# Kernel tuning notes

Hardware: AMD Instinct MI355X
Metric: run time of the kernel (lower is better)

The kernel has to match this reference:

```python
import jax, jax.numpy as jnp
import numpy as np

C_FEAT = 512
HID = 256
OUT = 3
IN_DIM = C_FEAT + 2 + 2  # feat + rel_coord + rel_cell = 516


def _nearest_idx(g, size):
    # grid_sample nearest, align_corners=False: unnormalize then round (half-to-even)
    x = ((g + 1.0) * size - 1.0) / 2.0
    return jnp.clip(jnp.round(x).astype(jnp.int32), 0, size - 1)


def setup_inputs() -> dict:
    key = jax.random.key(0)
    ks = jax.random.split(key, 12)
    B, Q, H, W = 2, 65536, 48, 48
    feat = jax.random.normal(ks[0], (B, C_FEAT, H, W), dtype=jnp.float32)
    coord = jax.random.uniform(ks[1], (B, Q, 2), dtype=jnp.float32, minval=-1.0, maxval=1.0)
    cell = jnp.full((B, Q, 2), 2.0 / 256.0, dtype=jnp.float32)  # query at 256x256 output res
    def lin_init(k, fan_in, fan_out):
        s = 1.0 / np.sqrt(fan_in)
        return jax.random.uniform(k, (fan_in, fan_out), jnp.float32, -s, s)
    W0 = lin_init(ks[2], IN_DIM, HID); b0 = jnp.zeros((HID,), jnp.float32)
    W1 = lin_init(ks[3], HID, HID);    b1 = jnp.zeros((HID,), jnp.float32)
    W2 = lin_init(ks[4], HID, HID);    b2 = jnp.zeros((HID,), jnp.float32)
    W3 = lin_init(ks[5], HID, HID);    b3 = jnp.zeros((HID,), jnp.float32)
    W4 = lin_init(ks[6], HID, OUT);    b4 = jnp.zeros((OUT,), jnp.float32)
    return {"feat": feat, "coord": coord, "cell": cell,
            "W0": W0, "b0": b0, "W1": W1, "b1": b1, "W2": W2, "b2": b2,
            "W3": W3, "b3": b3, "W4": W4, "b4": b4}


def _liif(feat, coord, cell, W0, b0, W1, b1, W2, b2, W3, b3, W4, b4):
    B, C, H, W = feat.shape
    Q = coord.shape[1]
    rx = 1.0 / H  # 2 / H / 2
    ry = 1.0 / W
    eps = 1e-6
    # local ensemble shifts (vx, vy) in order [(-1,-1),(-1,1),(1,-1),(1,1)]
    shifts = jnp.array([[-1., -1.], [-1., 1.], [1., -1.], [1., 1.]], dtype=feat.dtype)
    off = shifts * jnp.array([rx, ry], dtype=feat.dtype) + eps  # [4,2]
    coord_s = jnp.clip(coord[None] + off[:, None, None, :], -1 + 1e-6, 1 - 1e-6)  # [4,B,Q,2]
    # coord[...,0] indexes H (rows), coord[...,1] indexes W (cols) [code flips before grid_sample]
    idx_r = _nearest_idx(coord_s[..., 0], H)  # [4,B,Q]
    idx_c = _nearest_idx(coord_s[..., 1], W)
    lin = idx_r * W + idx_c                   # [4,B,Q]
    flat = feat.reshape(B, C, H * W).transpose(0, 2, 1)  # [B,HW,C]
    q_feat = jnp.take_along_axis(flat[None], lin[..., None], axis=2)  # [4,B,Q,C]
    # feat_coord grid_sample == center coord of the gathered cell
    qc_r = (idx_r.astype(feat.dtype) + 0.5) * (2.0 / H) - 1.0
    qc_c = (idx_c.astype(feat.dtype) + 0.5) * (2.0 / W) - 1.0
    rel = jnp.stack([(coord[None, ..., 0] - qc_r) * H,
                     (coord[None, ..., 1] - qc_c) * W], axis=-1)  # [4,B,Q,2]
    rel_cell = cell * jnp.array([H, W], dtype=feat.dtype)          # [B,Q,2]
    rel_cell4 = jnp.broadcast_to(rel_cell[None], (4, B, Q, 2))
    inp = jnp.concatenate([q_feat, rel, rel_cell4], axis=-1)       # [4,B,Q,516]
    # shared per-point MLP
    h = jax.nn.relu(inp @ W0 + b0)
    h = jax.nn.relu(h @ W1 + b1)
    h = jax.nn.relu(h @ W2 + b2)
    h = jax.nn.relu(h @ W3 + b3)
    pred = h @ W4 + b4                                             # [4,B,Q,3]
    area = jnp.abs(rel[..., 0] * rel[..., 1]) + 1e-9               # [4,B,Q]
    tot = area.sum(axis=0)
    # swap areas 0<->3 and 1<->2 (diagonal weighting) == reverse
    w = area[::-1] / tot[None]
    return (pred * w[..., None]).sum(axis=0)                       # [B,Q,3]


def reference(feat, coord, cell, W0, b0, W1, b1, W2, b2, W3, b3, W4, b4):
    return _liif(feat, coord, cell, W0, b0, W1, b1, W2, b2, W3, b3, W4, b4)
```

## Files before the change

### kernel.cpp

```cpp
#include <hip/hip_runtime.h>
#include <hip/hip_bf16.h>
#include <math.h>

#define HH    48
#define CFEAT 512
#define HID   256
#define NPOS  (HH*HH)
#define TQ    64
#define NEV   256

typedef __attribute__((ext_vector_type(8))) short bf16x8;
typedef __attribute__((ext_vector_type(4))) float f32x4;

static __device__ __forceinline__ unsigned short f2bf(float x) {
  unsigned int u = __float_as_uint(x);
  u += 0x7fffu + ((u >> 16) & 1u);
  return (unsigned short)(u >> 16);
}

static __device__ __forceinline__ unsigned int pk2bf(float a, float b) {
  __hip_bfloat162 h2 = __float22bfloat162_rn(make_float2(a, b));
  unsigned int u; __builtin_memcpy(&u, &h2, 4); return u;
}

static __device__ __forceinline__ void rel_calc(float c0, float c1, int s,
                                                float& r0, float& r1,
                                                int& ir, int& ic) {
  float vx = (s & 2) ? 1.0f : -1.0f;
  float vy = (s & 1) ? 1.0f : -1.0f;
  const float RXY = (float)(1.0/48.0);
  const float CLO = (float)(-1.0 + 1e-6);
  const float CHI = (float)( 1.0 - 1e-6);
  float gx = __fadd_rn(c0, __fadd_rn(__fmul_rn(vx, RXY), 1e-6f));
  float gy = __fadd_rn(c1, __fadd_rn(__fmul_rn(vy, RXY), 1e-6f));
  gx = fminf(fmaxf(gx, CLO), CHI);
  gy = fminf(fmaxf(gy, CLO), CHI);
  float xr = __fmul_rn(__fsub_rn(__fmul_rn(__fadd_rn(gx, 1.0f), 48.0f), 1.0f), 0.5f);
  float xc = __fmul_rn(__fsub_rn(__fmul_rn(__fadd_rn(gy, 1.0f), 48.0f), 1.0f), 0.5f);
  ir = (int)rintf(xr); ir = ir < 0 ? 0 : (ir > HH-1 ? HH-1 : ir);
  ic = (int)rintf(xc); ic = ic < 0 ? 0 : (ic > HH-1 ? HH-1 : ic);
  const float T2 = (float)(2.0/48.0);
  float qcr = __fsub_rn(__fmul_rn(__fadd_rn((float)ir, 0.5f), T2), 1.0f);
  float qcc = __fsub_rn(__fmul_rn(__fadd_rn((float)ic, 0.5f), T2), 1.0f);
  r0 = __fmul_rn(__fsub_rn(c0, qcr), 48.0f);
  r1 = __fmul_rn(__fsub_rn(c1, qcc), 48.0f);
}

__global__ __launch_bounds__(256) void liif_precompute(
    const float* __restrict__ feat, const float* __restrict__ W0,
    const float* __restrict__ b0, float* __restrict__ P)
{
  int blk = blockIdx.x;
  int b   = blk / (NPOS/4);
  int p0  = (blk - b*(NPOS/4)) * 4;
  int n   = threadIdx.x;
  const float* f = feat + (size_t)b * CFEAT * NPOS + p0;
  float bias = b0[n];
  float a0 = bias, a1 = bias, a2 = bias, a3 = bias;
  #pragma unroll 4
  for (int c = 0; c < CFEAT; ++c) {
    float w = W0[c*HID + n];
    const float* fr = f + (size_t)c * NPOS;
    a0 += fr[0]*w; a1 += fr[1]*w; a2 += fr[2]*w; a3 += fr[3]*w;
  }
  float* Pp = P + ((size_t)b*NPOS + p0)*HID + n;
  Pp[0*HID] = a0; Pp[1*HID] = a1; Pp[2*HID] = a2; Pp[3*HID] = a3;
}

__global__ __launch_bounds__(256) void liif_convert(
    const float* __restrict__ W1, const float* __restrict__ W2,
    const float* __restrict__ W3, const float* __restrict__ W4,
    unsigned char* __restrict__ img, unsigned char* __restrict__ w4i)
{
  int blk = blockIdx.x, t = threadIdx.x;
  if (blk < 24) {
    int l = blk >> 3, kc = blk & 7;
    const float* W = (l == 0) ? W1 : (l == 1) ? W2 : W3;
    unsigned short* dst = (unsigned short*)(img + (size_t)blk * 16384);
    #pragma unroll 1
    for (int s = 0; s < 4; ++s) {
      int p    = t + s*256;
      int wc   = p >> 8;
      int nt   = (p >> 6) & 3;
      int lane = p & 63;
      int lr   = lane & 15, lk = lane >> 4;
      int n    = wc*64 + nt*16 + lr;
      int k0   = kc*32 + lk*8;
      #pragma unroll
      for (int j = 0; j < 8; ++j)
        dst[p*8 + j] = f2bf(W[(k0 + j)*256 + n]);
    }
  } else {
    unsigned short* dst = (unsigned short*)w4i;
    #pragma unroll
    for (int u = 0; u < 2; ++u) {
      int p    = t + u*256;
      int kc   = p >> 6;
      int lane = p & 63;
      int n    = lane & 15;
      int k0   = kc*32 + (lane >> 4)*8;
      #pragma unroll
      for (int j = 0; j < 8; ++j)
        dst[p*8 + j] = (n < 3) ? f2bf(W4[(k0 + j)*3 + n]) : (unsigned short)0;
    }
  }
}


#define LDSW   131072

#define MF(A, B, C) __builtin_amdgcn_mfma_f32_16x16x32_bf16((A), (B), (C), 0, 0, 0)

#define AS1(p) ((const __attribute__((address_space(1))) void*)(unsigned long long)(const void*)(p))
#define AS3(p) ((__attribute__((address_space(3))) void*)(unsigned int)(unsigned long long)(void*)(p))

#define STAGE2(LOFF, NKC, BUF) do {                                           \
    __builtin_amdgcn_global_load_lds(                                         \
        AS1(img + (LOFF) + (NKC)*16384 + sgoff),                              \
        AS3(lds + LDSW + (BUF)*16384 + swoff), 16, 0, 0);                     \
    __builtin_amdgcn_global_load_lds(                                         \
        AS1(img + (LOFF) + (NKC)*16384 + sgoff + 8192),                       \
        AS3(lds + LDSW + (BUF)*16384 + swoff + 8192), 16, 0, 0);              \
  } while (0)

#define KSTEP32(KC, HASN, NLOFF, NKC) do {                                    \
    if (HASN) STAGE2((NLOFF), (NKC), (((KC)+1)&1));                           \
    const unsigned char* wb_ = lds + LDSW + (((KC)&1)*16384) + lwoff;         \
    bf16x8 w0_ = *(const bf16x8*)(wb_ + 0);                                   \
    bf16x8 w1_ = *(const bf16x8*)(wb_ + 1024);                                \
    bf16x8 w2_ = *(const bf16x8*)(wb_ + 2048);                                \
    bf16x8 w3_ = *(const bf16x8*)(wb_ + 3072);                                \
    bf16x8 w4_ = *(const bf16x8*)(wb_ + 4096);                                \
    bf16x8 w5_ = *(const bf16x8*)(wb_ + 5120);                                \
    bf16x8 w6_ = *(const bf16x8*)(wb_ + 6144);                                \
    bf16x8 w7_ = *(const bf16x8*)(wb_ + 7168);                                \
    const int ko_ = (((KC) << 6) ^ xb6);                                      \
    bf16x8 a0_ = *(const bf16x8*)(lds + rb0 + ko_);                           \
    bf16x8 a1_ = *(const bf16x8*)(lds + rb1 + ko_);                           \
    bf16x8 a2_ = *(const bf16x8*)(lds + rb2 + ko_);                           \
    bf16x8 a3_ = *(const bf16x8*)(lds + rb3 + ko_);                           \
    acc[0]  = MF(w0_, a0_, acc[0]);  acc[1]  = MF(w1_, a0_, acc[1]);          \
    acc[2]  = MF(w2_, a0_, acc[2]);  acc[3]  = MF(w3_, a0_, acc[3]);          \
    acc[4]  = MF(w4_, a0_, acc[4]);  acc[5]  = MF(w5_, a0_, acc[5]);          \
    acc[6]  = MF(w6_, a0_, acc[6]);  acc[7]  = MF(w7_, a0_, acc[7]);          \
    acc[8]  = MF(w0_, a1_, acc[8]);  acc[9]  = MF(w1_, a1_, acc[9]);          \
    acc[10] = MF(w2_, a1_, acc[10]); acc[11] = MF(w3_, a1_, acc[11]);         \
    acc[12] = MF(w4_, a1_, acc[12]); acc[13] = MF(w5_, a1_, acc[13]);         \
    acc[14] = MF(w6_, a1_, acc[14]); acc[15] = MF(w7_, a1_, acc[15]);         \
    acc[16] = MF(w0_, a2_, acc[16]); acc[17] = MF(w1_, a2_, acc[17]);         \
    acc[18] = MF(w2_, a2_, acc[18]); acc[19] = MF(w3_, a2_, acc[19]);         \
    acc[20] = MF(w4_, a2_, acc[20]); acc[21] = MF(w5_, a2_, acc[21]);         \
    acc[22] = MF(w6_, a2_, acc[22]); acc[23] = MF(w7_, a2_, acc[23]);         \
    acc[24] = MF(w0_, a3_, acc[24]); acc[25] = MF(w1_, a3_, acc[25]);         \
    acc[26] = MF(w2_, a3_, acc[26]); acc[27] = MF(w3_, a3_, acc[27]);         \
    acc[28] = MF(w4_, a3_, acc[28]); acc[29] = MF(w5_, a3_, acc[29]);         \
    acc[30] = MF(w6_, a3_, acc[30]); acc[31] = MF(w7_, a3_, acc[31]);         \
    __syncthreads();                                                          \
  } while (0)

#define LAYER32(LOFF, NLOFF) do {                                             \
    _Pragma("unroll")                                                         \
    for (int i_ = 0; i_ < 32; ++i_) acc[i_] = (f32x4){0.f, 0.f, 0.f, 0.f};    \
    KSTEP32(0, 1, (LOFF), 1); KSTEP32(1, 1, (LOFF), 2);                       \
    KSTEP32(2, 1, (LOFF), 3); KSTEP32(3, 1, (LOFF), 4);                       \
    KSTEP32(4, 1, (LOFF), 5); KSTEP32(5, 1, (LOFF), 6);                       \
    KSTEP32(6, 1, (LOFF), 7); KSTEP32(7, 1, (NLOFF), 0);                      \
  } while (0)

#define LAYER_WB(BIAS) do {                                                   \
    _Pragma("unroll")                                                         \
    for (int nt_ = 0; nt_ < 8; ++nt_) {                                       \
      f32x4 bv_ = *(const f32x4*)&(BIAS)[nW + nt_*16 + lk*4];                 \
      const int cb_ = (cwb + nt_*32) ^ xwb;                                   \
      _Pragma("unroll")                                                       \
      for (int mt_ = 0; mt_ < 4; ++mt_) {                                     \
        f32x4 a_ = acc[mt_*8 + nt_];                                          \
        unsigned int lo_ = pk2bf(fmaxf(a_[0] + bv_[0], 0.f),                  \
                                 fmaxf(a_[1] + bv_[1], 0.f));                 \
        unsigned int hi_ = pk2bf(fmaxf(a_[2] + bv_[2], 0.f),                  \
                                 fmaxf(a_[3] + bv_[3], 0.f));                 \
        *(uint2*)(lds + ((m0 + mt_*16 + lr) << 9) + cb_) = make_uint2(lo_, hi_); \
      }                                                                       \
    }                                                                         \
  } while (0)

__global__ __launch_bounds__(512, 2)
__attribute__((amdgpu_waves_per_eu(2, 2)))
void liif_main(
    const float* __restrict__ coord, const float* __restrict__ cell,
    const float* __restrict__ P,  const float* __restrict__ W0,
    const unsigned char* __restrict__ img,
    const unsigned char* __restrict__ w4i,
    const float* __restrict__ b1, const float* __restrict__ b2,
    const float* __restrict__ b3, const float* __restrict__ b4,
    float* __restrict__ out)
{
  __shared__ __align__(16) unsigned char lds[163840];
  int*   lin_s = (int*)  (lds + 147456);
  f32x4* rel4  = (f32x4*)(lds + 147456 + 1024);
  float* predp = (float*)lds;

  const int t   = threadIdx.x;
  const int blk = blockIdx.x;
  const int b   = blk >> 10;
  const int q0  = (blk & 1023) * TQ;

  const int lane = t & 63;
  const int w    = t >> 6;
  const int m0   = (w >> 1) * 64;
  const int nW   = (w & 1) * 128;
  const int lr   = lane & 15;
  const int lk   = lane >> 4;

  const size_t sgoff = (size_t)t * 16;
  const int    swoff = w * 1024;

  const int lwoff = (w & 1)*8192 + lane*16;
  const int xl  = (lr & 3) << 4;
  const int xb6 = ((lr >> 2) & 1) << 6;
  const int rb0 = ((m0 +  0 + lr) << 9) + ((lk << 4) ^ xl);
  const int rb1 = ((m0 + 16 + lr) << 9) + ((lk << 4) ^ xl);
  const int rb2 = ((m0 + 32 + lr) << 9) + ((lk << 4) ^ xl);
  const int rb3 = ((m0 + 48 + lr) << 9) + ((lk << 4) ^ xl);
  const int cwb = (w & 1)*256 + lk*8;
  const int xwb = (lr & 7) << 4;

  if (t < NEV) {
    const int e = t;
    const int q = q0 + (e >> 2);
    const int s = e & 3;
    const size_t cbase = (((size_t)b << 16) + q) * 2;
    float c0 = coord[cbase + 0];
    float c1 = coord[cbase + 1];
    float r0, r1; int ir, ic;
    rel_calc(c0, c1, s, r0, r1, ir, ic);
    lin_s[e] = ir*HH + ic;
    rel4[e] = (f32x4){r0, r1,
                      __fmul_rn(cell[cbase + 0], 48.0f),
                      __fmul_rn(cell[cbase + 1], 48.0f)};
  }
  __syncthreads();

  STAGE2(0, 0, 0);

  {
    const int cg = lane;
    const float* w0t = W0 + (size_t)512*HID + cg*4;
    f32x4 wr0 = *(const f32x4*)(w0t);
    f32x4 wr1 = *(const f32x4*)(w0t + 256);
    f32x4 wr2 = *(const f32x4*)(w0t + 512);
    f32x4 wr3 = *(const f32x4*)(w0t + 768);
    const float* Pb = P + (size_t)b * NPOS * HID + cg*4;
    const int wb = cg * 8;
    #pragma unroll 2
    for (int i = 0; i < 32; ++i) {
      const int e = w*32 + i;
      const int lin = lin_s[e];
      f32x4 rel = rel4[e];
      f32x4 pv = *(const f32x4*)(Pb + (size_t)lin*HID);
      float v0 = pv[0] + rel[0]*wr0[0] + rel[1]*wr1[0] + rel[2]*wr2[0] + rel[3]*wr3[0];
      float v1 = pv[1] + rel[0]*wr0[1] + rel[1]*wr1[1] + rel[2]*wr2[1] + rel[3]*wr3[1];
      float v2 = pv[2] + rel[0]*wr0[2] + rel[1]*wr1[2] + rel[2]*wr2[2] + rel[3]*wr3[2];
      float v3 = pv[3] + rel[0]*wr0[3] + rel[1]*wr1[3] + rel[2]*wr2[3] + rel[3]*wr3[3];
      unsigned int lo = pk2bf(fmaxf(v0, 0.f), fmaxf(v1, 0.f));
      unsigned int hi = pk2bf(fmaxf(v2, 0.f), fmaxf(v3, 0.f));
      *(uint2*)(lds + (e << 9) + (wb ^ ((e & 7) << 4))) = make_uint2(lo, hi);
    }
  }
  __syncthreads();

  f32x4 acc[32];
  LAYER32(0, 131072);
  LAYER_WB(b1);
  __syncthreads();

  LAYER32(131072, 262144);
  LAYER_WB(b2);
  __syncthreads();

  {
    #pragma unroll
    for (int i_ = 0; i_ < 32; ++i_) acc[i_] = (f32x4){0.f, 0.f, 0.f, 0.f};
    KSTEP32(0, 1, 262144, 1); KSTEP32(1, 1, 262144, 2);
    KSTEP32(2, 1, 262144, 3); KSTEP32(3, 1, 262144, 4);
    KSTEP32(4, 1, 262144, 5); KSTEP32(5, 1, 262144, 6);
    KSTEP32(6, 1, 262144, 7);
    __builtin_amdgcn_global_load_lds(AS1(w4i + sgoff),
                                     AS3(lds + LDSW + swoff), 16, 0, 0);
    KSTEP32(7, 0, 0, 0);
  }
  LAYER_WB(b3);
  __syncthreads();

  {
    f32x4 acc4a = (f32x4){0.f, 0.f, 0.f, 0.f};
    f32x4 acc4b = (f32x4){0.f, 0.f, 0.f, 0.f};
    const int fr0 = ((w*32)      + lr) << 9;
    const int fr1 = ((w*32 + 16) + lr) << 9;
    #pragma unroll
    for (int kc = 0; kc < 8; ++kc) {
      bf16x8 wf = *(const bf16x8*)(lds + LDSW + kc*1024 + lane*16);
      const int ko = ((kc << 6) ^ xb6) + ((lk << 4) ^ xl);
      bf16x8 afa = *(const bf16x8*)(lds + fr0 + ko);
      bf16x8 afb = *(const bf16x8*)(lds + fr1 + ko);
      acc4a = MF(wf, afa, acc4a);
      acc4b = MF(wf, afb, acc4b);
    }
    __syncthreads();
    if (lk == 0) {
      float* pa = predp + (w*32 + lr)*3;
      float* pb = predp + (w*32 + 16 + lr)*3;
      pa[0] = acc4a[0] + b4[0]; pa[1] = acc4a[1] + b4[1]; pa[2] = acc4a[2] + b4[2];
      pb[0] = acc4b[0] + b4[0]; pb[1] = acc4b[1] + b4[1]; pb[2] = acc4b[2] + b4[2];
    }
  }
  __syncthreads();

  if (t < TQ*3) {
    const int q = t / 3, o = t - (t/3)*3;
    const int eb = q*4;
    const size_t cbase = (((size_t)b << 16) + (q0 + q)) * 2;
    float c0 = coord[cbase + 0];
    float c1 = coord[cbase + 1];
    float ar[4];
    #pragma unroll
    for (int s = 0; s < 4; ++s) {
      float r0, r1; int ir, ic;
      rel_calc(c0, c1, s, r0, r1, ir, ic);
      ar[s] = __fadd_rn(fabsf(__fmul_rn(r0, r1)), 1e-9f);
    }
    float p0 = predp[(eb+0)*3 + o];
    float p1 = predp[(eb+1)*3 + o];
    float p2 = predp[(eb+2)*3 + o];
    float p3 = predp[(eb+3)*3 + o];
    float tot = ((ar[0] + ar[1]) + ar[2]) + ar[3];
    float rv = (p0*ar[3] + p1*ar[2] + p2*ar[1] + p3*ar[0]) / tot;
    out[(((size_t)b << 16) + (q0 + q))*3 + o] = rv;
  }
}

extern "C" void kernel_launch(void* const* d_in, const int* in_sizes, int n_in,
                              void* d_out, int out_size, void* d_ws, size_t ws_size,
                              hipStream_t stream)
{
  const float* feat  = (const float*)d_in[0];
  const float* coord = (const float*)d_in[1];
  const float* cell  = (const float*)d_in[2];
  const float* W0    = (const float*)d_in[3];
  const float* b0    = (const float*)d_in[4];
  const float* W1    = (const float*)d_in[5];
  const float* b1    = (const float*)d_in[6];
  const float* W2    = (const float*)d_in[7];
  const float* b2    = (const float*)d_in[8];
  const float* W3    = (const float*)d_in[9];
  const float* b3    = (const float*)d_in[10];
  const float* W4    = (const float*)d_in[11];
  const float* b4    = (const float*)d_in[12];
  float* outp = (float*)d_out;

  float*         P    = (float*)d_ws;
  unsigned char* imgp = (unsigned char*)d_ws + 4718592;
  unsigned char* w4ip = (unsigned char*)d_ws + 4718592 + 393216;

  hipLaunchKernelGGL(liif_precompute, dim3(2*(NPOS/4)), dim3(256), 0, stream,
                     feat, W0, b0, P);
  hipLaunchKernelGGL(liif_convert, dim3(25), dim3(256), 0, stream,
                     W1, W2, W3, W4, imgp, w4ip);
  hipLaunchKernelGGL(liif_main, dim3(2048), dim3(512), 0, stream,
                     coord, cell, P, W0, imgp, w4ip, b1, b2, b3, b4, outp);
}
```

Baseline: 298.4 us.

## Halve threads per block, enlarge per-wave tiles, and software-pipeline MLP k-steps

The main kernel now runs 256 threads per block with one wave per EU, and each wave computes a 128x128 output tile (64 accumulators) instead of 64x128. Weight chunks are double-buffered further ahead: each chunk is staged two k-steps early, and LDS reads for the next k-step are issued before the MFMAs of the current one. MFMA bursts run at raised priority via s_setprio. The intent is to reuse each operand fragment across more MFMAs and hide LDS and global latency. The cost is much higher register pressure and half the waves per CU for latency hiding.

```diff
diff --git a/kernel.cpp b/kernel.cpp
--- a/kernel.cpp
+++ b/kernel.cpp
@@ -114,57 +114,33 @@
 #define AS1(p) ((const __attribute__((address_space(1))) void*)(unsigned long long)(const void*)(p))
 #define AS3(p) ((__attribute__((address_space(3))) void*)(unsigned int)(unsigned long long)(void*)(p))
 
-#define STAGE2(LOFF, NKC, BUF) do {                                           \
-    __builtin_amdgcn_global_load_lds(                                         \
-        AS1(img + (LOFF) + (NKC)*16384 + sgoff),                              \
-        AS3(lds + LDSW + (BUF)*16384 + swoff), 16, 0, 0);                     \
-    __builtin_amdgcn_global_load_lds(                                         \
-        AS1(img + (LOFF) + (NKC)*16384 + sgoff + 8192),                       \
-        AS3(lds + LDSW + (BUF)*16384 + swoff + 8192), 16, 0, 0);              \
-  } while (0)
-
-#define KSTEP32(KC, HASN, NLOFF, NKC) do {                                    \
-    if (HASN) STAGE2((NLOFF), (NKC), (((KC)+1)&1));                           \
-    const unsigned char* wb_ = lds + LDSW + (((KC)&1)*16384) + lwoff;         \
-    bf16x8 w0_ = *(const bf16x8*)(wb_ + 0);                                   \
-    bf16x8 w1_ = *(const bf16x8*)(wb_ + 1024);                                \
-    bf16x8 w2_ = *(const bf16x8*)(wb_ + 2048);                                \
-    bf16x8 w3_ = *(const bf16x8*)(wb_ + 3072);                                \
-    bf16x8 w4_ = *(const bf16x8*)(wb_ + 4096);                                \
-    bf16x8 w5_ = *(const bf16x8*)(wb_ + 5120);                                \
-    bf16x8 w6_ = *(const bf16x8*)(wb_ + 6144);                                \
-    bf16x8 w7_ = *(const bf16x8*)(wb_ + 7168);                                \
-    const int ko_ = (((KC) << 6) ^ xb6);                                      \
-    bf16x8 a0_ = *(const bf16x8*)(lds + rb0 + ko_);                           \
-    bf16x8 a1_ = *(const bf16x8*)(lds + rb1 + ko_);                           \
-    bf16x8 a2_ = *(const bf16x8*)(lds + rb2 + ko_);                           \
-    bf16x8 a3_ = *(const bf16x8*)(lds + rb3 + ko_);                           \
-    acc[0]  = MF(w0_, a0_, acc[0]);  acc[1]  = MF(w1_, a0_, acc[1]);          \
-    acc[2]  = MF(w2_, a0_, acc[2]);  acc[3]  = MF(w3_, a0_, acc[3]);          \
-    acc[4]  = MF(w4_, a0_, acc[4]);  acc[5]  = MF(w5_, a0_, acc[5]);          \
-    acc[6]  = MF(w6_, a0_, acc[6]);  acc[7]  = MF(w7_, a0_, acc[7]);          \
-    acc[8]  = MF(w0_, a1_, acc[8]);  acc[9]  = MF(w1_, a1_, acc[9]);          \
-    acc[10] = MF(w2_, a1_, acc[10]); acc[11] = MF(w3_, a1_, acc[11]);         \
-    acc[12] = MF(w4_, a1_, acc[12]); acc[13] = MF(w5_, a1_, acc[13]);         \
-    acc[14] = MF(w6_, a1_, acc[14]); acc[15] = MF(w7_, a1_, acc[15]);         \
-    acc[16] = MF(w0_, a2_, acc[16]); acc[17] = MF(w1_, a2_, acc[17]);         \
-    acc[18] = MF(w2_, a2_, acc[18]); acc[19] = MF(w3_, a2_, acc[19]);         \
-    acc[20] = MF(w4_, a2_, acc[20]); acc[21] = MF(w5_, a2_, acc[21]);         \
-    acc[22] = MF(w6_, a2_, acc[22]); acc[23] = MF(w7_, a2_, acc[23]);         \
-    acc[24] = MF(w0_, a3_, acc[24]); acc[25] = MF(w1_, a3_, acc[25]);         \
-    acc[26] = MF(w2_, a3_, acc[26]); acc[27] = MF(w3_, a3_, acc[27]);         \
-    acc[28] = MF(w4_, a3_, acc[28]); acc[29] = MF(w5_, a3_, acc[29]);         \
-    acc[30] = MF(w6_, a3_, acc[30]); acc[31] = MF(w7_, a3_, acc[31]);         \
-    __syncthreads();                                                          \
-  } while (0)
-
-#define LAYER32(LOFF, NLOFF) do {                                             \
-    _Pragma("unroll")                                                         \
-    for (int i_ = 0; i_ < 32; ++i_) acc[i_] = (f32x4){0.f, 0.f, 0.f, 0.f};    \
-    KSTEP32(0, 1, (LOFF), 1); KSTEP32(1, 1, (LOFF), 2);                       \
-    KSTEP32(2, 1, (LOFF), 3); KSTEP32(3, 1, (LOFF), 4);                       \
-    KSTEP32(4, 1, (LOFF), 5); KSTEP32(5, 1, (LOFF), 6);                       \
-    KSTEP32(6, 1, (LOFF), 7); KSTEP32(7, 1, (NLOFF), 0);                      \
+#define STAGE4(LOFF, KC, BUF) do {                                            \
+    _Pragma("unroll")                                                         \
+    for (int j_ = 0; j_ < 4; ++j_)                                            \
+      __builtin_amdgcn_global_load_lds(                                       \
+          AS1(img + (LOFF) + (KC)*16384 + sgoff + j_*4096),                   \
+          AS3(lds + LDSW + (BUF)*16384 + j_*4096 + swoff), 16, 0, 0);         \
+  } while (0)
+
+#define RD(AARR, WARR, KC) do {                                               \
+    const unsigned char* wbp_ = lds + LDSW + (((KC)&1)*16384) + lwoff;        \
+    _Pragma("unroll")                                                         \
+    for (int j_ = 0; j_ < 8; ++j_)                                            \
+      WARR[j_] = *(const bf16x8*)(wbp_ + j_*1024);                            \
+    const int ko_ = (((KC) << 6) ^ xb6) + ((lk << 4) ^ xl);                   \
+    _Pragma("unroll")                                                         \
+    for (int m_ = 0; m_ < 8; ++m_)                                            \
+      AARR[m_] = *(const bf16x8*)(lds + ((m0 + m_*16 + lr) << 9) + ko_);      \
+  } while (0)
+
+#define MM(WARR, AARR) do {                                                   \
+    __builtin_amdgcn_s_setprio(1);                                            \
+    _Pragma("unroll")                                                         \
+    for (int m_ = 0; m_ < 8; ++m_)                                            \
+      _Pragma("unroll")                                                       \
+      for (int n_ = 0; n_ < 8; ++n_)                                          \
+        acc[m_*8 + n_] = MF(WARR[n_], AARR[m_], acc[m_*8 + n_]);              \
+    __builtin_amdgcn_s_setprio(0);                                            \
   } while (0)
 
 #define LAYER_WB(BIAS) do {                                                   \
@@ -173,7 +149,7 @@
       f32x4 bv_ = *(const f32x4*)&(BIAS)[nW + nt_*16 + lk*4];                 \
       const int cb_ = (cwb + nt_*32) ^ xwb;                                   \
       _Pragma("unroll")                                                       \
-      for (int mt_ = 0; mt_ < 4; ++mt_) {                                     \
+      for (int mt_ = 0; mt_ < 8; ++mt_) {                                     \
         f32x4 a_ = acc[mt_*8 + nt_];                                          \
         unsigned int lo_ = pk2bf(fmaxf(a_[0] + bv_[0], 0.f),                  \
                                  fmaxf(a_[1] + bv_[1], 0.f));                 \
@@ -184,8 +160,34 @@
     }                                                                         \
   } while (0)
 
-__global__ __launch_bounds__(512, 2)
-__attribute__((amdgpu_waves_per_eu(2, 2)))
+#define LAYER128(LOFF, NLOFF, ISL3) do {                                      \
+    RD(aE, wE, 0);                                                            \
+    _Pragma("unroll")                                                         \
+    for (int i_ = 0; i_ < 64; ++i_) acc[i_] = (f32x4){0.f, 0.f, 0.f, 0.f};    \
+    __syncthreads(); STAGE4((LOFF), 2, 0); RD(aO, wO, 1); MM(wE, aE);   \
+    __syncthreads(); STAGE4((LOFF), 3, 1); RD(aE, wE, 2); MM(wO, aO);   \
+    __syncthreads(); STAGE4((LOFF), 4, 0); RD(aO, wO, 3); MM(wE, aE);   \
+    __syncthreads(); STAGE4((LOFF), 5, 1); RD(aE, wE, 4); MM(wO, aO);   \
+    __syncthreads(); STAGE4((LOFF), 6, 0); RD(aO, wO, 5); MM(wE, aE);   \
+    __syncthreads(); STAGE4((LOFF), 7, 1); RD(aE, wE, 6); MM(wO, aO);   \
+    __syncthreads();                                                    \
+    if (ISL3) {                                                               \
+      _Pragma("unroll")                                                       \
+      for (int j_ = 0; j_ < 2; ++j_)                                          \
+        __builtin_amdgcn_global_load_lds(                                     \
+            AS1(w4i + sgoff + j_*4096),                                       \
+            AS3(lds + LDSW + j_*4096 + swoff), 16, 0, 0);                     \
+    } else {                                                                  \
+      STAGE4((NLOFF), 0, 0);                                                  \
+    }                                                                         \
+    RD(aO, wO, 7); MM(wE, aE);                                                \
+    __syncthreads();                                                    \
+    if (!(ISL3)) STAGE4((NLOFF), 1, 1);                                       \
+    MM(wO, aO);                                                               \
+  } while (0)
+
+__global__ __launch_bounds__(256, 1)
+__attribute__((amdgpu_waves_per_eu(1, 1)))
 void liif_main(
     const float* __restrict__ coord, const float* __restrict__ cell,
     const float* __restrict__ P,  const float* __restrict__ W0,
@@ -207,7 +209,7 @@
 
   const int lane = t & 63;
   const int w    = t >> 6;
-  const int m0   = (w >> 1) * 64;
+  const int m0   = (w >> 1) * 128;
   const int nW   = (w & 1) * 128;
   const int lr   = lane & 15;
   const int lk   = lane >> 4;
@@ -218,10 +220,6 @@
   const int lwoff = (w & 1)*8192 + lane*16;
   const int xl  = (lr & 3) << 4;
   const int xb6 = ((lr >> 2) & 1) << 6;
-  const int rb0 = ((m0 +  0 + lr) << 9) + ((lk << 4) ^ xl);
-  const int rb1 = ((m0 + 16 + lr) << 9) + ((lk << 4) ^ xl);
-  const int rb2 = ((m0 + 32 + lr) << 9) + ((lk << 4) ^ xl);
-  const int rb3 = ((m0 + 48 + lr) << 9) + ((lk << 4) ^ xl);
   const int cwb = (w & 1)*256 + lk*8;
   const int xwb = (lr & 7) << 4;
 
@@ -241,7 +239,7 @@
   }
   __syncthreads();
 
-  STAGE2(0, 0, 0);
+  STAGE4(0, 0, 0);
 
   {
     const int cg = lane;
@@ -252,9 +250,9 @@
     f32x4 wr3 = *(const f32x4*)(w0t + 768);
     const float* Pb = P + (size_t)b * NPOS * HID + cg*4;
     const int wb = cg * 8;
-    #pragma unroll 2
-    for (int i = 0; i < 32; ++i) {
-      const int e = w*32 + i;
+    #pragma unroll 4
+    for (int i = 0; i < 64; ++i) {
+      const int e = w*64 + i;
       const int lin = lin_s[e];
       f32x4 rel = rel4[e];
       f32x4 pv = *(const f32x4*)(Pb + (size_t)lin*HID);
@@ -269,49 +267,46 @@
   }
   __syncthreads();
 
-  f32x4 acc[32];
-  LAYER32(0, 131072);
+  STAGE4(0, 1, 1);
+
+  f32x4 acc[64];
+  bf16x8 wE[8], aE[8], wO[8], aO[8];
+
+  LAYER128(0, 131072, 0);
   LAYER_WB(b1);
   __syncthreads();
 
-  LAYER32(131072, 262144);
+  LAYER128(131072, 262144, 0);
   LAYER_WB(b2);
   __syncthreads();
 
+  LAYER128(262144, 0, 1);
+  LAYER_WB(b3);
+  __syncthreads();
+
   {
+    f32x4 acc4[4];
     #pragma unroll
-    for (int i_ = 0; i_ < 32; ++i_) acc[i_] = (f32x4){0.f, 0.f, 0.f, 0.f};
-    KSTEP32(0, 1, 262144, 1); KSTEP32(1, 1, 262144, 2);
-    KSTEP32(2, 1, 262144, 3); KSTEP32(3, 1, 262144, 4);
-    KSTEP32(4, 1, 262144, 5); KSTEP32(5, 1, 262144, 6);
-    KSTEP32(6, 1, 262144, 7);
-    __builtin_amdgcn_global_load_lds(AS1(w4i + sgoff),
-                                     AS3(lds + LDSW + swoff), 16, 0, 0);
-    KSTEP32(7, 0, 0, 0);
-  }
-  LAYER_WB(b3);
-  __syncthreads();
-
-  {
-    f32x4 acc4a = (f32x4){0.f, 0.f, 0.f, 0.f};
-    f32x4 acc4b = (f32x4){0.f, 0.f, 0.f, 0.f};
-    const int fr0 = ((w*32)      + lr) << 9;
-    const int fr1 = ((w*32 + 16) + lr) << 9;
+    for (int g = 0; g < 4; ++g) acc4[g] = (f32x4){0.f, 0.f, 0.f, 0.f};
     #pragma unroll
     for (int kc = 0; kc < 8; ++kc) {
       bf16x8 wf = *(const bf16x8*)(lds + LDSW + kc*1024 + lane*16);
       const int ko = ((kc << 6) ^ xb6) + ((lk << 4) ^ xl);
-      bf16x8 afa = *(const bf16x8*)(lds + fr0 + ko);
-      bf16x8 afb = *(const bf16x8*)(lds + fr1 + ko);
-      acc4a = MF(wf, afa, acc4a);
-      acc4b = MF(wf, afb, acc4b);
+      #pragma unroll
+      for (int g = 0; g < 4; ++g) {
+        bf16x8 af = *(const bf16x8*)(lds + ((w*64 + g*16 + lr) << 9) + ko);
+        acc4[g] = MF(wf, af, acc4[g]);
+      }
     }
     __syncthreads();
     if (lk == 0) {
-      float* pa = predp + (w*32 + lr)*3;
-      float* pb = predp + (w*32 + 16 + lr)*3;
-      pa[0] = acc4a[0] + b4[0]; pa[1] = acc4a[1] + b4[1]; pa[2] = acc4a[2] + b4[2];
-      pb[0] = acc4b[0] + b4[0]; pb[1] = acc4b[1] + b4[1]; pb[2] = acc4b[2] + b4[2];
+      #pragma unroll
+      for (int g = 0; g < 4; ++g) {
+        float* pp = predp + (w*64 + g*16 + lr)*3;
+        pp[0] = acc4[g][0] + b4[0];
+        pp[1] = acc4[g][1] + b4[1];
+        pp[2] = acc4[g][2] + b4[2];
+      }
     }
   }
   __syncthreads();
@@ -366,6 +361,6 @@
                      feat, W0, b0, P);
   hipLaunchKernelGGL(liif_convert, dim3(25), dim3(256), 0, stream,
                      W1, W2, W3, W4, imgp, w4ip);
-  hipLaunchKernelGGL(liif_main, dim3(2048), dim3(512), 0, stream,
+  hipLaunchKernelGGL(liif_main, dim3(2048), dim3(256), 0, stream,
                      coord, cell, P, W0, imgp, w4ip, b1, b2, b3, b4, outp);
 }
```

Measured after the change: 367.3 us. +23.1%, slower.
